# Performance work log

Hardware: AMD Instinct MI355X
Metric: run time of the kernel (lower is better)

Reference implementation:

```python
import jax, jax.numpy as jnp
import numpy as np

N = 8192
NFEAT = 64
OUT = 64


def setup_inputs() -> dict:
    key = jax.random.key(0)
    ks = jax.random.split(key, 7)
    A_stack = jax.random.uniform(ks[0], (N, N, 5), dtype=jnp.float32)
    feature = jax.random.normal(ks[1], (N, NFEAT), dtype=jnp.float32)
    weight_b = jax.random.uniform(ks[2], (5, 1), dtype=jnp.float32) * 0.1
    stdv1 = 1.0 / np.sqrt(OUT)
    W1 = jax.random.uniform(ks[3], (NFEAT, OUT), dtype=jnp.float32, minval=-stdv1, maxval=stdv1)
    b1 = jax.random.uniform(ks[4], (OUT,), dtype=jnp.float32, minval=-stdv1, maxval=stdv1)
    W2 = jax.random.uniform(ks[5], (OUT, OUT), dtype=jnp.float32, minval=-stdv1, maxval=stdv1)
    b2 = jax.random.uniform(ks[6], (OUT,), dtype=jnp.float32, minval=-stdv1, maxval=stdv1)
    return {"A_stack": A_stack, "feature": feature, "weight_b": weight_b,
            "W1": W1, "b1": b1, "W2": W2, "b2": b2}


def reference(A_stack, feature, weight_b, W1, b1, W2, b2):
    # Multiplex relation aggregation: weighted sum of 5 adjacency layers, then symmetrize.
    temp = jnp.einsum('ijk,kl->ij', A_stack, weight_b)  # [N, N]
    final_A = temp + temp.T
    # GCN layer 1: spmm(adj, X @ W1) + b1
    U1 = final_A @ (feature @ W1) + b1
    # GCN layer 2
    U2 = final_A @ (U1 @ W2) + b2
    return (U1 + U2) * 0.5
```

## Files before the change

kernel.cpp:

```cpp
#include <hip/hip_runtime.h>
#include <hip/hip_bf16.h>


#define NN 8192

typedef __attribute__((ext_vector_type(8))) short short8;
typedef __attribute__((ext_vector_type(8))) unsigned short u16x8;
typedef __attribute__((ext_vector_type(4))) unsigned short u16x4;
typedef __attribute__((ext_vector_type(4))) float f32x4;

static __device__ __forceinline__ unsigned short f2bf(float f) {
    unsigned u = __float_as_uint(f);
    u += 0x7FFFu + ((u >> 16) & 1u);
    return (unsigned short)(u >> 16);
}

#define GL16(gsrc, ldst) __builtin_amdgcn_global_load_lds( \
    (const __attribute__((address_space(1))) void*)(gsrc), \
    (__attribute__((address_space(3))) void*)(ldst), 16, 0, 0)

__global__ __launch_bounds__(256) void k_sym_build(
        const float* __restrict__ A, const float* __restrict__ wb,
        unsigned short* __restrict__ S) {
    __shared__ float Raw[2][16 * 320];
    __shared__ float T1s[64 * 65];
    __shared__ float T2t[64 * 65];

    int b = blockIdx.x;
    double disc = 66049.0 - 8.0 * (double)b;
    int bi = (int)((257.0 - sqrt(disc)) * 0.5);
    if (bi < 0) bi = 0; if (bi > 127) bi = 127;
    while (bi < 127 && (bi + 1) * (257 - (bi + 1)) / 2 <= b) ++bi;
    while (bi > 0 && bi * (257 - bi) / 2 > b) --bi;
    int bj = bi + (b - bi * (257 - bi) / 2);

    const float w0 = wb[0], w1 = wb[1], w2 = wb[2], w3 = wb[3], w4 = wb[4];
    int t = threadIdx.x;

    int srow[5], srem[5];
    #pragma unroll
    for (int q = 0; q < 5; ++q) {
        int o = t * 16 + q * 4096;
        srow[q] = o / 1280;
        srem[q] = (o % 1280) >> 2;
    }
    int cr = t >> 4;
    int cj = t & 15;

    auto stage = [&](int k, int buf) {
        int half = k >> 2, bat = k & 3;
        int tr = half == 0 ? bi : bj;
        int tc = half == 0 ? bj : bi;
        #pragma unroll
        for (int q = 0; q < 5; ++q) {
            const float* src = A +
                ((long long)(tr * 64 + bat * 16 + srow[q]) * NN + tc * 64) * 5
                + srem[q];
            GL16(src, (char*)&Raw[buf][0] + t * 16 + q * 4096);
        }
    };

    stage(0, 0);
    for (int k = 0; k < 8; ++k) {
        int cur = k & 1;
        asm volatile("s_waitcnt vmcnt(0)" ::: "memory");
        __builtin_amdgcn_s_barrier();
        __builtin_amdgcn_sched_barrier(0);
        if (k < 7) stage(k + 1, cur ^ 1);
        int half = k >> 2;
        int gr = (k & 3) * 16 + cr;
        #pragma unroll
        for (int e = 0; e < 4; ++e) {
            int j = cj + 16 * e;
            const float* p = &Raw[cur][cr * 320 + 5 * j];
            float tv = p[0]*w0 + p[1]*w1 + p[2]*w2 + p[3]*w3 + p[4]*w4;
            if (half == 0) T1s[gr * 65 + j] = tv;
            else           T2t[j * 65 + gr] = tv;
        }
    }
    __syncthreads();

    #pragma unroll
    for (int e = 0; e < 2; ++e) {
        int i = (t >> 3) + 32 * e;
        int j0 = (t & 7) * 8;
        u16x8 o;
        #pragma unroll
        for (int q = 0; q < 8; ++q)
            o[q] = f2bf(T1s[i * 65 + j0 + q] + T2t[i * 65 + j0 + q]);
        *(u16x8*)(S + (long long)(bi * 64 + i) * NN + bj * 64 + j0) = o;
    }
    if (bi != bj) {
        #pragma unroll
        for (int e = 0; e < 2; ++e) {
            int i = (t >> 3) + 32 * e;
            int j0 = (t & 7) * 8;
            u16x8 o;
            #pragma unroll
            for (int q = 0; q < 8; ++q)
                o[q] = f2bf(T1s[(j0 + q) * 65 + i] + T2t[(j0 + q) * 65 + i]);
            *(u16x8*)(S + (long long)(bj * 64 + i) * NN + bi * 64 + j0) = o;
        }
    }
}

__global__ __launch_bounds__(256) void k_small_gemm_t(
        const float* __restrict__ X, const float* __restrict__ W,
        unsigned short* __restrict__ Yt) {
    __shared__ float Ys[64 * 65];
    int t = threadIdx.x, lane = t & 63, w = t >> 6;
    float wcol[64];
    #pragma unroll
    for (int k = 0; k < 64; ++k) wcol[k] = W[k * 64 + lane];
    int r0 = blockIdx.x * 64;
    for (int rr = 0; rr < 16; ++rr) {
        const f32x4* x = (const f32x4*)(X + (long long)(r0 + w * 16 + rr) * 64);
        float acc = 0.f;
        #pragma unroll
        for (int k4 = 0; k4 < 16; ++k4) {
            f32x4 xv = x[k4];
            acc += xv[0]*wcol[4*k4] + xv[1]*wcol[4*k4+1]
                 + xv[2]*wcol[4*k4+2] + xv[3]*wcol[4*k4+3];
        }
        Ys[lane * 65 + w * 16 + rr] = acc;
    }
    __syncthreads();
    int c = t >> 2, j0 = (t & 3) * 16;
    u16x8 o0, o1;
    #pragma unroll
    for (int q = 0; q < 8; ++q) {
        o0[q] = f2bf(Ys[c * 65 + j0 + q]);
        o1[q] = f2bf(Ys[c * 65 + j0 + 8 + q]);
    }
    *(u16x8*)(Yt + (long long)c * NN + r0 + j0) = o0;
    *(u16x8*)(Yt + (long long)c * NN + r0 + j0 + 8) = o1;
}

template<int FINAL>
__global__ __launch_bounds__(256) void k_gemm_skinny(
        const unsigned short* __restrict__ S,
        const unsigned short* __restrict__ Ht,
        const float* __restrict__ bias,
        const float* __restrict__ U1,
        float* __restrict__ Y) {
    __shared__ unsigned short Ts[2][16 * 128];
    __shared__ unsigned short Hs[2][64 * 128];
    int t = threadIdx.x, lane = t & 63, w = t >> 6;
    int i0 = blockIdx.x * 16;
    int r = lane & 15, kg = lane >> 4;

    int srow = t >> 4, sc = t & 15;
    int sbyte = (sc * 16) ^ ((srow & 7) << 4);
    const unsigned short* aSrc = S + (long long)(i0 + srow) * NN + (sbyte >> 1);
    const unsigned short* hSrc = Ht + (long long)srow * NN + (sbyte >> 1);
    char* tsDst0 = (char*)&Ts[0][0] + t * 16;
    char* tsDst1 = (char*)&Ts[1][0] + t * 16;
    char* hsDst0 = (char*)&Hs[0][0] + t * 16;
    char* hsDst1 = (char*)&Hs[1][0] + t * 16;

    f32x4 acc = {0.f, 0.f, 0.f, 0.f};

    GL16(aSrc, tsDst0);
    #pragma unroll
    for (int q = 0; q < 4; ++q)
        GL16(hSrc + (long long)q * 16 * NN, hsDst0 + q * 4096);
    __syncthreads();

    int cur = 0;
    for (int jt = 0; jt < NN; jt += 128) {
        if (jt + 128 < NN) {
            if (cur == 0) {
                GL16(aSrc + jt + 128, tsDst1);
                #pragma unroll
                for (int q = 0; q < 4; ++q)
                    GL16(hSrc + (long long)q * 16 * NN + jt + 128, hsDst1 + q * 4096);
            } else {
                GL16(aSrc + jt + 128, tsDst0);
                #pragma unroll
                for (int q = 0; q < 4; ++q)
                    GL16(hSrc + (long long)q * 16 * NN + jt + 128, hsDst0 + q * 4096);
            }
        }
        const char* tsB = (const char*)&Ts[cur][0];
        const char* hsB = (const char*)&Hs[cur][0];
        int hr = w * 16 + r;
        #pragma unroll
        for (int kk = 0; kk < 4; ++kk) {
            int xo = kk * 64 + kg * 16;
            short8 a = *(const short8*)(tsB + r * 256 + (xo ^ ((r & 7) << 4)));
            short8 bb = *(const short8*)(hsB + hr * 256 + (xo ^ ((r & 7) << 4)));
            acc = __builtin_amdgcn_mfma_f32_16x16x32_bf16(a, bb, acc, 0, 0, 0);
        }
        __syncthreads();
        cur ^= 1;
    }

    int f = w * 16 + r;
    float bv = bias[f];
    #pragma unroll
    for (int rr = 0; rr < 4; ++rr) {
        long long gi = (long long)(i0 + kg * 4 + rr) * 64 + f;
        float v = acc[rr] + bv;
        if (FINAL) v = 0.5f * (U1[gi] + v);
        Y[gi] = v;
    }
}

extern "C" void kernel_launch(void* const* d_in, const int* in_sizes, int n_in,
                              void* d_out, int out_size, void* d_ws, size_t ws_size,
                              hipStream_t stream) {
    const float* A    = (const float*)d_in[0];
    const float* feat = (const float*)d_in[1];
    const float* wb   = (const float*)d_in[2];
    const float* W1   = (const float*)d_in[3];
    const float* b1   = (const float*)d_in[4];
    const float* W2   = (const float*)d_in[5];
    const float* b2   = (const float*)d_in[6];
    float* out = (float*)d_out;

    const size_t szS = (size_t)NN * NN * 2;
    const size_t szH = (size_t)64 * NN * 2;
    char* p = (char*)d_ws;
    unsigned short* S   = (unsigned short*)p;
    unsigned short* H1t = (unsigned short*)(p + szS);
    unsigned short* H2t = (unsigned short*)(p + szS + szH);
    float*          U1  = (float*)(p + szS + 2 * szH);

    k_sym_build<<<8256, 256, 0, stream>>>(A, wb, S);
    k_small_gemm_t<<<128, 256, 0, stream>>>(feat, W1, H1t);
    k_gemm_skinny<0><<<512, 256, 0, stream>>>(S, H1t, b1, nullptr, U1);
    k_small_gemm_t<<<128, 256, 0, stream>>>(U1, W2, H2t);
    k_gemm_skinny<1><<<512, 256, 0, stream>>>(S, H2t, b2, U1, out);
}
```

Baseline: 425.8 us.

## Deepen skinny GEMM load pipeline to four LDS stages with partial vmcnt waits

Replaces the double-buffered skinny GEMM main loop with a four-slot LDS ring that keeps three tiles of async global-to-LDS loads in flight. Each iteration waits with a partial vmcnt so only the oldest tile must have landed, which removes the trailing __syncthreads per iteration and hides more memory latency. It doubles LDS use per block (to about 80KB), which may reduce how many blocks fit per CU.

```diff
diff --git a/kernel.cpp b/kernel.cpp
--- a/kernel.cpp
+++ b/kernel.cpp
@@ -143,8 +143,8 @@
         const float* __restrict__ bias,
         const float* __restrict__ U1,
         float* __restrict__ Y) {
-    __shared__ unsigned short Ts[2][16 * 128];
-    __shared__ unsigned short Hs[2][64 * 128];
+    __shared__ unsigned short Ts[4][16 * 128];
+    __shared__ unsigned short Hs[4][64 * 128];
     int t = threadIdx.x, lane = t & 63, w = t >> 6;
     int i0 = blockIdx.x * 16;
     int r = lane & 15, kg = lane >> 4;
@@ -153,37 +153,20 @@
     int sbyte = (sc * 16) ^ ((srow & 7) << 4);
     const unsigned short* aSrc = S + (long long)(i0 + srow) * NN + (sbyte >> 1);
     const unsigned short* hSrc = Ht + (long long)srow * NN + (sbyte >> 1);
-    char* tsDst0 = (char*)&Ts[0][0] + t * 16;
-    char* tsDst1 = (char*)&Ts[1][0] + t * 16;
-    char* hsDst0 = (char*)&Hs[0][0] + t * 16;
-    char* hsDst1 = (char*)&Hs[1][0] + t * 16;
 
     f32x4 acc = {0.f, 0.f, 0.f, 0.f};
-
-    GL16(aSrc, tsDst0);
-    #pragma unroll
-    for (int q = 0; q < 4; ++q)
-        GL16(hSrc + (long long)q * 16 * NN, hsDst0 + q * 4096);
-    __syncthreads();
-
-    int cur = 0;
-    for (int jt = 0; jt < NN; jt += 128) {
-        if (jt + 128 < NN) {
-            if (cur == 0) {
-                GL16(aSrc + jt + 128, tsDst1);
-                #pragma unroll
-                for (int q = 0; q < 4; ++q)
-                    GL16(hSrc + (long long)q * 16 * NN + jt + 128, hsDst1 + q * 4096);
-            } else {
-                GL16(aSrc + jt + 128, tsDst0);
-                #pragma unroll
-                for (int q = 0; q < 4; ++q)
-                    GL16(hSrc + (long long)q * 16 * NN + jt + 128, hsDst0 + q * 4096);
-            }
-        }
-        const char* tsB = (const char*)&Ts[cur][0];
-        const char* hsB = (const char*)&Hs[cur][0];
-        int hr = w * 16 + r;
+    int hr = w * 16 + r;
+
+    auto stage = [&](int tile, int d) {
+        GL16(aSrc + tile * 128, (char*)&Ts[d][0] + t * 16);
+        #pragma unroll
+        for (int q = 0; q < 4; ++q)
+            GL16(hSrc + (long long)q * 16 * NN + tile * 128,
+                 (char*)&Hs[d][0] + t * 16 + q * 4096);
+    };
+    auto compute = [&](int k) {
+        const char* tsB = (const char*)&Ts[k & 3][0];
+        const char* hsB = (const char*)&Hs[k & 3][0];
         #pragma unroll
         for (int kk = 0; kk < 4; ++kk) {
             int xo = kk * 64 + kg * 16;
@@ -191,9 +174,28 @@
             short8 bb = *(const short8*)(hsB + hr * 256 + (xo ^ ((r & 7) << 4)));
             acc = __builtin_amdgcn_mfma_f32_16x16x32_bf16(a, bb, acc, 0, 0, 0);
         }
-        __syncthreads();
-        cur ^= 1;
-    }
+    };
+
+    stage(0, 0); stage(1, 1); stage(2, 2);
+    for (int k = 0; k < 61; ++k) {
+        asm volatile("s_waitcnt vmcnt(10)" ::: "memory");
+        __builtin_amdgcn_s_barrier();
+        __builtin_amdgcn_sched_barrier(0);
+        stage(k + 3, (k + 3) & 3);
+        compute(k);
+    }
+    asm volatile("s_waitcnt vmcnt(10)" ::: "memory");
+    __builtin_amdgcn_s_barrier();
+    __builtin_amdgcn_sched_barrier(0);
+    compute(61);
+    asm volatile("s_waitcnt vmcnt(5)" ::: "memory");
+    __builtin_amdgcn_s_barrier();
+    __builtin_amdgcn_sched_barrier(0);
+    compute(62);
+    asm volatile("s_waitcnt vmcnt(0)" ::: "memory");
+    __builtin_amdgcn_s_barrier();
+    __builtin_amdgcn_sched_barrier(0);
+    compute(63);
 
     int f = w * 16 + r;
     float bv = bias[f];
```

Result: no change. 434.1 us (+2.0%).
